# Performance work log

Hardware: AMD Instinct MI355X
Metric: run time of the kernel (lower is better)

The kernel has to match this reference:

```python
import jax, jax.numpy as jnp
import numpy as np

B, N, C, K, D = 32, 4096, 37, 100, 512   # images, rois, classes(incl bg), max dets/class, feat dim
C1 = C - 1
SCORE_TH, NMS_TH = 0.1, 0.4
BBOX_STDS = jnp.array([0.1, 0.1, 0.2, 0.2], jnp.float32)
HS, WS, SCALE = 960.0, 1280.0, 1.6  # scaled image height/width, resize scale


def setup_inputs() -> dict:
    key = jax.random.key(0)
    k1, k2, k3, k4 = jax.random.split(key, 4)
    u = jax.random.uniform(k1, (B, N, 4))
    x1 = u[..., 0] * (WS - 160.0)
    y1 = u[..., 1] * (HS - 160.0)
    w = u[..., 2] * 140.0 + 20.0
    h = u[..., 3] * 140.0 + 20.0
    boxes = jnp.stack([x1, y1, x1 + w, y1 + h], -1)          # [B,N,4] in scaled coords
    box_deltas = jax.random.normal(k2, (B, N, 4 * C)) * 0.5   # [B,N,4C]
    scores = jax.nn.softmax(jax.random.normal(k3, (B, N, C)) * 2.0, axis=-1)  # [B,N,C]
    roi_features = jax.random.normal(k4, (B, N, D))           # [B,N,D]
    im_info = jnp.tile(jnp.array([[HS, WS, SCALE]], jnp.float32), (B, 1))     # [B,3]
    return dict(boxes=boxes, box_deltas=box_deltas, scores=scores,
                roi_features=roi_features, im_info=im_info)


def _decode_clip(boxes, deltas, im_info):
    # bbox_transform_inv with normalize stds, then clip_boxes, then /scale.
    d = deltas.reshape(B, N, C, 4) * BBOX_STDS                # [B,N,C,4]
    w = boxes[..., 2] - boxes[..., 0] + 1.0
    h = boxes[..., 3] - boxes[..., 1] + 1.0
    cx = boxes[..., 0] + 0.5 * w
    cy = boxes[..., 1] + 0.5 * h
    pcx = d[..., 0] * w[..., None] + cx[..., None]
    pcy = d[..., 1] * h[..., None] + cy[..., None]
    pw = jnp.exp(d[..., 2]) * w[..., None]
    ph = jnp.exp(d[..., 3]) * h[..., None]
    hmax = im_info[:, 0][:, None, None] - 1.0
    wmax = im_info[:, 1][:, None, None] - 1.0
    x1 = jnp.clip(pcx - 0.5 * pw, 0.0, wmax)
    y1 = jnp.clip(pcy - 0.5 * ph, 0.0, hmax)
    x2 = jnp.clip(pcx + 0.5 * pw, 0.0, wmax)
    y2 = jnp.clip(pcy + 0.5 * ph, 0.0, hmax)
    pred = jnp.stack([x1, y1, x2, y2], -1)                    # [B,N,C,4]
    return pred / im_info[:, 2][:, None, None, None]


def _pairwise_iou(b):
    # b: [K,4] -> [K,K]
    area = (b[:, 2] - b[:, 0]) * (b[:, 3] - b[:, 1])
    lt = jnp.maximum(b[:, None, :2], b[None, :, :2])
    rb = jnp.minimum(b[:, None, 2:], b[None, :, 2:])
    wh = jnp.clip(rb - lt, 0.0)
    inter = wh[..., 0] * wh[..., 1]
    return inter / (area[:, None] + area[None, :] - inter + 1e-8)


def _nms_one_class(cls_boxes, cls_scores, feats):
    # cls_boxes [N,4], cls_scores [N], feats [N,D] -> det [K, 4+1+D]
    s = jnp.where(cls_scores > SCORE_TH, cls_scores, -1.0)
    vals, idx = jax.lax.top_k(s, K)                           # sorted desc == torch.sort(desc)
    b = cls_boxes[idx]                                        # [K,4]
    ious = _pairwise_iou(b)                                   # [K,K]
    valid = vals > SCORE_TH
    rng = jnp.arange(K)

    def body(i, keep):
        sup = (ious[i] > NMS_TH) & (rng > i) & keep[i]
        return keep & ~sup

    keep = jax.lax.fori_loop(0, K, body, valid)               # greedy NMS, fixed size
    det = jnp.concatenate([b, vals[:, None], feats[idx]], -1)  # [K,5+D]
    return jnp.where(keep[:, None], det, 0.0)


def reference(boxes, box_deltas, scores, roi_features, im_info):
    pred = _decode_clip(boxes, box_deltas, im_info)           # [B,N,C,4]
    cls_boxes = pred[:, :, 1:, :]                             # drop background, [B,N,C1,4]
    cls_scores = scores[:, :, 1:]                             # [B,N,C1]
    per_image = jax.vmap(_nms_one_class, in_axes=(1, 1, None))  # over class axis
    per_batch = jax.vmap(per_image, in_axes=(0, 0, 0))          # over image axis
    return per_batch(cls_boxes, cls_scores, roi_features)     # [B,C1,K,5+D]
```

## Files before the change

### kernel.cpp

```cpp
#include <hip/hip_runtime.h>
#include <cmath>

#define BB 32
#define NN 4096
#define NC 37
#define C1 36
#define KK 100
#define DD 512
#define SCORE_TH 0.1f
#define NMS_TH 0.4f
#define CAND_CAP 4096
#define NT 256

__global__ __launch_bounds__(NT) void detect_kernel(
    const float* __restrict__ boxes,
    const float* __restrict__ deltas,
    const float* __restrict__ scores,
    const float* __restrict__ feats,
    const float* __restrict__ im_info,
    float* __restrict__ out)
{
#pragma clang fp contract(off)
    __shared__ unsigned long long cand[CAND_CAP];
    __shared__ int cnt;
    __shared__ float sbox[KK][4];
    __shared__ float sarea[KK];
    __shared__ float sval[KK];
    __shared__ int   sidx[KK];
    __shared__ int   skeep[KK];

    const int bc  = blockIdx.x;
    const int b   = bc / C1;
    const int c   = bc % C1;
    const int tid = threadIdx.x;

    if (tid == 0) cnt = 0;
    __syncthreads();

    for (int n = tid; n < NN; n += NT) {
        float v = scores[(b * NN + n) * NC + (c + 1)];
        if (v > SCORE_TH) {
            int pos = atomicAdd(&cnt, 1);
            unsigned int vb = __float_as_uint(v);
            cand[pos] = ((unsigned long long)vb << 32) | (unsigned int)(0xFFFFFFFFu - (unsigned int)n);
        }
    }
    __syncthreads();
    const int M = cnt;

    int P = 128;
    while (P < M) P <<= 1;
    for (int i = M + tid; i < P; i += NT) cand[i] = 0ULL;
    __syncthreads();

    for (int k = 2; k <= P; k <<= 1) {
        for (int j = k >> 1; j > 0; j >>= 1) {
            for (int i = tid; i < P; i += NT) {
                int ixj = i ^ j;
                if (ixj > i) {
                    unsigned long long a  = cand[i];
                    unsigned long long bb = cand[ixj];
                    bool desc = ((i & k) == 0);
                    if (desc ? (a < bb) : (a > bb)) {
                        cand[i]   = bb;
                        cand[ixj] = a;
                    }
                }
            }
            __syncthreads();
        }
    }

    const int V = (M < KK) ? M : KK;

    if (tid < KK) {
        int k = tid;
        if (k < V) {
            unsigned long long key = cand[k];
            float v = __uint_as_float((unsigned int)(key >> 32));
            int   n = (int)(0xFFFFFFFFu - (unsigned int)(key & 0xFFFFFFFFull));
            sval[k] = v;
            sidx[k] = n;
            skeep[k] = 1;

            const float* bp = boxes + (b * NN + n) * 4;
            float bx1 = bp[0], by1 = bp[1], bx2 = bp[2], by2 = bp[3];
            const float* dp = deltas + ((b * NN + n) * NC + (c + 1)) * 4;
            float d0 = dp[0] * 0.1f;
            float d1 = dp[1] * 0.1f;
            float d2 = dp[2] * 0.2f;
            float d3 = dp[3] * 0.2f;

            float w  = bx2 - bx1 + 1.0f;
            float h  = by2 - by1 + 1.0f;
            float cx = bx1 + 0.5f * w;
            float cy = by1 + 0.5f * h;
            float pcx = d0 * w + cx;
            float pcy = d1 * h + cy;
            float pw  = (float)exp((double)d2) * w;
            float ph  = (float)exp((double)d3) * h;

            float hmax = im_info[b * 3 + 0] - 1.0f;
            float wmax = im_info[b * 3 + 1] - 1.0f;
            float sc   = im_info[b * 3 + 2];

            float x1p = fminf(fmaxf(pcx - 0.5f * pw, 0.0f), wmax);
            float y1p = fminf(fmaxf(pcy - 0.5f * ph, 0.0f), hmax);
            float x2p = fminf(fmaxf(pcx + 0.5f * pw, 0.0f), wmax);
            float y2p = fminf(fmaxf(pcy + 0.5f * ph, 0.0f), hmax);
            x1p = x1p / sc; y1p = y1p / sc; x2p = x2p / sc; y2p = y2p / sc;

            sbox[k][0] = x1p; sbox[k][1] = y1p; sbox[k][2] = x2p; sbox[k][3] = y2p;
            sarea[k] = (x2p - x1p) * (y2p - y1p);
        } else {
            sval[k] = 0.0f; sidx[k] = 0; skeep[k] = 0;
            sbox[k][0] = sbox[k][1] = sbox[k][2] = sbox[k][3] = 0.0f;
            sarea[k] = 0.0f;
        }
    }
    __syncthreads();

    for (int i = 0; i < V; ++i) {
        if (tid < KK && tid > i && skeep[i] && skeep[tid]) {
            float ax1 = sbox[i][0], ay1 = sbox[i][1], ax2 = sbox[i][2], ay2 = sbox[i][3];
            float qx1 = sbox[tid][0], qy1 = sbox[tid][1], qx2 = sbox[tid][2], qy2 = sbox[tid][3];
            float ltx = fmaxf(ax1, qx1);
            float lty = fmaxf(ay1, qy1);
            float rbx = fminf(ax2, qx2);
            float rby = fminf(ay2, qy2);
            float iw = fmaxf(rbx - ltx, 0.0f);
            float ih = fmaxf(rby - lty, 0.0f);
            float inter = iw * ih;
            float denom = sarea[i] + sarea[tid];
            denom = denom - inter;
            denom = denom + 1e-8f;
            float iou = inter / denom;
            if (iou > NMS_TH) skeep[tid] = 0;
        }
        __syncthreads();
    }

    const int wv = tid >> 6;
    const int ln = tid & 63;
    const long long obase0 = (long long)bc * KK * 517;
    for (int k = wv; k < KK; k += (NT / 64)) {
        float* op = out + obase0 + (long long)k * 517;
        if (skeep[k]) {
            if (ln == 0) {
                __builtin_nontemporal_store(sbox[k][0], op + 0);
                __builtin_nontemporal_store(sbox[k][1], op + 1);
                __builtin_nontemporal_store(sbox[k][2], op + 2);
                __builtin_nontemporal_store(sbox[k][3], op + 3);
                __builtin_nontemporal_store(sval[k],    op + 4);
            }
            const float4* f4 = (const float4*)(feats + (long long)(b * NN + sidx[k]) * DD);
            float4 v0 = f4[ln];
            float4 v1 = f4[ln + 64];
            float* o5 = op + 5;
            const int j0 = ln * 4;
            __builtin_nontemporal_store(v0.x, o5 + j0 + 0);
            __builtin_nontemporal_store(v0.y, o5 + j0 + 1);
            __builtin_nontemporal_store(v0.z, o5 + j0 + 2);
            __builtin_nontemporal_store(v0.w, o5 + j0 + 3);
            const int j1 = (ln + 64) * 4;
            __builtin_nontemporal_store(v1.x, o5 + j1 + 0);
            __builtin_nontemporal_store(v1.y, o5 + j1 + 1);
            __builtin_nontemporal_store(v1.z, o5 + j1 + 2);
            __builtin_nontemporal_store(v1.w, o5 + j1 + 3);
        } else {
            #pragma unroll
            for (int t = 0; t < 8; ++t)
                __builtin_nontemporal_store(0.0f, op + t * 64 + ln);
            if (ln < 5)
                __builtin_nontemporal_store(0.0f, op + 512 + ln);
        }
    }
}

extern "C" void kernel_launch(void* const* d_in, const int* in_sizes, int n_in,
                              void* d_out, int out_size, void* d_ws, size_t ws_size,
                              hipStream_t stream) {
    const float* boxes    = (const float*)d_in[0];
    const float* deltas   = (const float*)d_in[1];
    const float* scores   = (const float*)d_in[2];
    const float* feats    = (const float*)d_in[3];
    const float* im_info  = (const float*)d_in[4];
    float* out = (float*)d_out;

    detect_kernel<<<dim3(BB * C1), dim3(NT), 0, stream>>>(
        boxes, deltas, scores, feats, im_info, out);
}
```

Baseline: 594.8 us.

## Split candidate scatter into separate kernel, chunked sort, wave-shuffle NMS, batched feature copy

Adds a zero kernel and a coalesced scatter kernel that reads scores once and bins above-threshold candidates per (image,class) into a workspace, replacing the strided per-block score reads. The detect kernel sorts candidates in chunks of a smaller shared buffer, keeping the top 100 between chunks. NMS now runs in a single wavefront using register shuffles instead of 100 block-wide barriers. The output write is restructured into a header pass and a per-wave feature copy loop with a branch-free zero path. The extra launches, global atomics and workspace traffic add overhead.

Result: slower. 753.4 us (+26.7%).

```diff
diff --git a/kernel.cpp b/kernel.cpp
--- a/kernel.cpp
+++ b/kernel.cpp
@@ -9,66 +9,99 @@
 #define DD 512
 #define SCORE_TH 0.1f
 #define NMS_TH 0.4f
-#define CAND_CAP 4096
+#define NBC (BB * C1)
+#define GCAP 4096
+#define LCAP 2048
 #define NT 256
+
+__global__ __launch_bounds__(256) void zero_kernel(int* __restrict__ gcnt)
+{
+    const int t = blockIdx.x * 256 + threadIdx.x;
+    if (t < NBC) gcnt[t] = 0;
+}
+
+__global__ __launch_bounds__(256) void scatter_kernel(
+    const float* __restrict__ scores,
+    int* __restrict__ gcnt,
+    unsigned long long* __restrict__ gcand)
+{
+    const int t = blockIdx.x * 256 + threadIdx.x;
+    const int TOT = BB * NN * NC;
+    if (t >= TOT) return;
+    float v = scores[t];
+    int c = t % NC;
+    if (c == 0) return;
+    if (v > SCORE_TH) {
+        int bn = t / NC;
+        int b = bn / NN;
+        int n = bn % NN;
+        int bc = b * C1 + (c - 1);
+        int pos = atomicAdd(&gcnt[bc], 1);
+        unsigned int vb = __float_as_uint(v);
+        gcand[(size_t)bc * GCAP + pos] =
+            ((unsigned long long)vb << 32) | (unsigned int)(0xFFFFFFFFu - (unsigned int)n);
+    }
+}
 
 __global__ __launch_bounds__(NT) void detect_kernel(
     const float* __restrict__ boxes,
     const float* __restrict__ deltas,
-    const float* __restrict__ scores,
     const float* __restrict__ feats,
     const float* __restrict__ im_info,
+    const int* __restrict__ gcnt,
+    const unsigned long long* __restrict__ gcand,
     float* __restrict__ out)
 {
 #pragma clang fp contract(off)
-    __shared__ unsigned long long cand[CAND_CAP];
-    __shared__ int cnt;
+    __shared__ unsigned long long cand[LCAP];
     __shared__ float sbox[KK][4];
     __shared__ float sarea[KK];
     __shared__ float sval[KK];
     __shared__ int   sidx[KK];
     __shared__ int   skeep[KK];
+    __shared__ unsigned int smeta[KK];
 
     const int bc  = blockIdx.x;
     const int b   = bc / C1;
     const int c   = bc % C1;
     const int tid = threadIdx.x;
 
-    if (tid == 0) cnt = 0;
-    __syncthreads();
-
-    for (int n = tid; n < NN; n += NT) {
-        float v = scores[(b * NN + n) * NC + (c + 1)];
-        if (v > SCORE_TH) {
-            int pos = atomicAdd(&cnt, 1);
-            unsigned int vb = __float_as_uint(v);
-            cand[pos] = ((unsigned long long)vb << 32) | (unsigned int)(0xFFFFFFFFu - (unsigned int)n);
-        }
-    }
-    __syncthreads();
-    const int M = cnt;
-
-    int P = 128;
-    while (P < M) P <<= 1;
-    for (int i = M + tid; i < P; i += NT) cand[i] = 0ULL;
-    __syncthreads();
-
-    for (int k = 2; k <= P; k <<= 1) {
-        for (int j = k >> 1; j > 0; j >>= 1) {
-            for (int i = tid; i < P; i += NT) {
-                int ixj = i ^ j;
-                if (ixj > i) {
-                    unsigned long long a  = cand[i];
-                    unsigned long long bb = cand[ixj];
-                    bool desc = ((i & k) == 0);
-                    if (desc ? (a < bb) : (a > bb)) {
-                        cand[i]   = bb;
-                        cand[ixj] = a;
+    const int M = gcnt[bc];
+    const unsigned long long* src = gcand + (size_t)bc * GCAP;
+
+    int take = M < LCAP ? M : LCAP;
+    for (int i = tid; i < take; i += NT) cand[i] = src[i];
+    int consumed = take;
+    int total    = take;
+
+    for (;;) {
+        int P = 128; while (P < total) P <<= 1;
+        for (int i = total + tid; i < P; i += NT) cand[i] = 0ULL;
+        __syncthreads();
+        for (int k = 2; k <= P; k <<= 1) {
+            for (int j = k >> 1; j > 0; j >>= 1) {
+                for (int i = tid; i < P; i += NT) {
+                    int ixj = i ^ j;
+                    if (ixj > i) {
+                        unsigned long long a  = cand[i];
+                        unsigned long long bb = cand[ixj];
+                        bool desc = ((i & k) == 0);
+                        if (desc ? (a < bb) : (a > bb)) {
+                            cand[i]   = bb;
+                            cand[ixj] = a;
+                        }
                     }
                 }
+                __syncthreads();
             }
-            __syncthreads();
-        }
+        }
+        if (consumed >= M) break;
+        int t2 = M - consumed;
+        if (t2 > LCAP - KK) t2 = LCAP - KK;
+        for (int i = tid; i < t2; i += NT) cand[KK + i] = src[consumed + i];
+        consumed += t2;
+        total = KK + t2;
+        __syncthreads();
     }
 
     const int V = (M < KK) ? M : KK;
@@ -120,60 +153,101 @@
     }
     __syncthreads();
 
-    for (int i = 0; i < V; ++i) {
-        if (tid < KK && tid > i && skeep[i] && skeep[tid]) {
-            float ax1 = sbox[i][0], ay1 = sbox[i][1], ax2 = sbox[i][2], ay2 = sbox[i][3];
-            float qx1 = sbox[tid][0], qy1 = sbox[tid][1], qx2 = sbox[tid][2], qy2 = sbox[tid][3];
-            float ltx = fmaxf(ax1, qx1);
-            float lty = fmaxf(ay1, qy1);
-            float rbx = fminf(ax2, qx2);
-            float rby = fminf(ay2, qy2);
-            float iw = fmaxf(rbx - ltx, 0.0f);
-            float ih = fmaxf(rby - lty, 0.0f);
-            float inter = iw * ih;
-            float denom = sarea[i] + sarea[tid];
-            denom = denom - inter;
-            denom = denom + 1e-8f;
-            float iou = inter / denom;
-            if (iou > NMS_TH) skeep[tid] = 0;
-        }
-        __syncthreads();
-    }
+    if (tid < 64) {
+        const int ln = tid;
+        float ax1 = sbox[ln][0], ay1 = sbox[ln][1], ax2 = sbox[ln][2], ay2 = sbox[ln][3];
+        float aar = sarea[ln];
+        int   ka  = (ln < V) ? 1 : 0;
+        float bx1 = 0.f, by1 = 0.f, bx2 = 0.f, by2 = 0.f, bar = 0.f;
+        int   kb  = 0;
+        if (ln < KK - 64) {
+            bx1 = sbox[64 + ln][0]; by1 = sbox[64 + ln][1];
+            bx2 = sbox[64 + ln][2]; by2 = sbox[64 + ln][3];
+            bar = sarea[64 + ln];
+            kb  = (64 + ln < V) ? 1 : 0;
+        }
+        for (int i = 0; i < V; ++i) {
+            const int  srcl = i & 63;
+            const bool hi   = (i >= 64);
+            int ki = __shfl(hi ? kb : ka, srcl);
+            if (ki) {
+                float ix1 = __shfl(hi ? bx1 : ax1, srcl);
+                float iy1 = __shfl(hi ? by1 : ay1, srcl);
+                float ix2 = __shfl(hi ? bx2 : ax2, srcl);
+                float iy2 = __shfl(hi ? by2 : ay2, srcl);
+                float iar = __shfl(hi ? bar : aar, srcl);
+                if (ka && ln > i) {
+                    float ltx = fmaxf(ix1, ax1);
+                    float lty = fmaxf(iy1, ay1);
+                    float rbx = fminf(ix2, ax2);
+                    float rby = fminf(iy2, ay2);
+                    float iw = fmaxf(rbx - ltx, 0.0f);
+                    float ih = fmaxf(rby - lty, 0.0f);
+                    float inter = iw * ih;
+                    float denom = iar + aar;
+                    denom = denom - inter;
+                    denom = denom + 1e-8f;
+                    if (inter / denom > NMS_TH) ka = 0;
+                }
+                if (kb && 64 + ln > i) {
+                    float ltx = fmaxf(ix1, bx1);
+                    float lty = fmaxf(iy1, by1);
+                    float rbx = fminf(ix2, bx2);
+                    float rby = fminf(iy2, by2);
+                    float iw = fmaxf(rbx - ltx, 0.0f);
+                    float ih = fmaxf(rby - lty, 0.0f);
+                    float inter = iw * ih;
+                    float denom = iar + bar;
+                    denom = denom - inter;
+                    denom = denom + 1e-8f;
+                    if (inter / denom > NMS_TH) kb = 0;
+                }
+            }
+        }
+        skeep[ln] = ka;
+        if (ln < KK - 64) skeep[64 + ln] = kb;
+    }
+    __syncthreads();
+
+    const long long bcbase = (long long)bc * (KK * 517);
+    for (int e = tid; e < KK; e += NT)
+        smeta[e] = skeep[e] ? (0x80000000u | (unsigned)sidx[e]) : 0u;
+    for (int e = tid; e < KK * 5; e += NT) {
+        int k = e / 5, j = e - k * 5;
+        float hv = (j < 4) ? sbox[k][j] : sval[k];
+        if (!skeep[k]) hv = 0.0f;
+        __builtin_nontemporal_store(hv, out + bcbase + (long long)k * 517 + j);
+    }
+    __syncthreads();
 
     const int wv = tid >> 6;
     const int ln = tid & 63;
-    const long long obase0 = (long long)bc * KK * 517;
-    for (int k = wv; k < KK; k += (NT / 64)) {
-        float* op = out + obase0 + (long long)k * 517;
-        if (skeep[k]) {
-            if (ln == 0) {
-                __builtin_nontemporal_store(sbox[k][0], op + 0);
-                __builtin_nontemporal_store(sbox[k][1], op + 1);
-                __builtin_nontemporal_store(sbox[k][2], op + 2);
-                __builtin_nontemporal_store(sbox[k][3], op + 3);
-                __builtin_nontemporal_store(sval[k],    op + 4);
-            }
-            const float4* f4 = (const float4*)(feats + (long long)(b * NN + sidx[k]) * DD);
-            float4 v0 = f4[ln];
-            float4 v1 = f4[ln + 64];
-            float* o5 = op + 5;
-            const int j0 = ln * 4;
-            __builtin_nontemporal_store(v0.x, o5 + j0 + 0);
-            __builtin_nontemporal_store(v0.y, o5 + j0 + 1);
-            __builtin_nontemporal_store(v0.z, o5 + j0 + 2);
-            __builtin_nontemporal_store(v0.w, o5 + j0 + 3);
-            const int j1 = (ln + 64) * 4;
-            __builtin_nontemporal_store(v1.x, o5 + j1 + 0);
-            __builtin_nontemporal_store(v1.y, o5 + j1 + 1);
-            __builtin_nontemporal_store(v1.z, o5 + j1 + 2);
-            __builtin_nontemporal_store(v1.w, o5 + j1 + 3);
-        } else {
-            #pragma unroll
-            for (int t = 0; t < 8; ++t)
-                __builtin_nontemporal_store(0.0f, op + t * 64 + ln);
-            if (ln < 5)
-                __builtin_nontemporal_store(0.0f, op + 512 + ln);
-        }
+    const int k0 = wv * 25;
+    int mym = (ln < 25) ? (int)smeta[k0 + ln] : 0;
+    const float* fbase = feats + (long long)b * NN * DD;
+#pragma unroll 2
+    for (int t = 0; t < 25; ++t) {
+        unsigned int m = (unsigned int)__shfl(mym, t);
+        const int  n  = (int)(m & 0x7FFFFFFFu);
+        const bool kp = (m & 0x80000000u) != 0u;
+        const float4* f4 = (const float4*)(fbase + (long long)n * DD);
+        float4 v0 = f4[ln];
+        float4 v1 = f4[ln + 64];
+        if (!kp) {
+            v0.x = v0.y = v0.z = v0.w = 0.0f;
+            v1.x = v1.y = v1.z = v1.w = 0.0f;
+        }
+        float* o5 = out + bcbase + (long long)(k0 + t) * 517 + 5;
+        const int j0 = ln * 4;
+        __builtin_nontemporal_store(v0.x, o5 + j0 + 0);
+        __builtin_nontemporal_store(v0.y, o5 + j0 + 1);
+        __builtin_nontemporal_store(v0.z, o5 + j0 + 2);
+        __builtin_nontemporal_store(v0.w, o5 + j0 + 3);
+        const int j1 = (ln + 64) * 4;
+        __builtin_nontemporal_store(v1.x, o5 + j1 + 0);
+        __builtin_nontemporal_store(v1.y, o5 + j1 + 1);
+        __builtin_nontemporal_store(v1.z, o5 + j1 + 2);
+        __builtin_nontemporal_store(v1.w, o5 + j1 + 3);
     }
 }
 
@@ -187,6 +261,15 @@
     const float* im_info  = (const float*)d_in[4];
     float* out = (float*)d_out;
 
-    detect_kernel<<<dim3(BB * C1), dim3(NT), 0, stream>>>(
-        boxes, deltas, scores, feats, im_info, out);
-}
+    char* ws = (char*)d_ws;
+    int* gcnt = (int*)ws;
+    unsigned long long* gcand =
+        (unsigned long long*)(ws + 8192);
+
+    zero_kernel<<<dim3((NBC + 255) / 256), dim3(256), 0, stream>>>(gcnt);
+
+    const int TOT = BB * NN * NC;
+    scatter_kernel<<<dim3((TOT + 255) / 256), dim3(256), 0, stream>>>(scores, gcnt, gcand);
+    detect_kernel<<<dim3(NBC), dim3(NT), 0, stream>>>(
+        boxes, deltas, feats, im_info, gcnt, gcand, out);
+}
```
